# Optimization experiments

Measured on AMD Instinct MI355X. Metric: run time of the kernel, lower is better.

Reference implementation:

```python
import jax, jax.numpy as jnp
import numpy as np

NU, NI = 100000, 50000      # global embedding table sizes
U, I = 50000, 20000         # nodes in this subgraph
E = 400000                  # edges per direction
HID, H = 512, 8
D = HID // H                # out_feats per head = 64
NEG_SLOPE = 0.2


def setup_inputs() -> dict:
    key = jax.random.key(0)
    ks = jax.random.split(key, 16)
    s = 1.0 / np.sqrt(HID)
    a = 1.0 / np.sqrt(D)
    return {
        'u_gid': jax.random.randint(ks[0], (U,), 0, NU),
        'i_gid': jax.random.randint(ks[1], (I,), 0, NI),
        'src_u': jax.random.randint(ks[2], (E,), 0, U),
        'dst_i': jax.random.randint(ks[3], (E,), 0, I),
        'user_emb': jax.random.normal(ks[4], (NU, HID), jnp.float32) * 0.02,
        'item_emb': jax.random.normal(ks[5], (NI, HID), jnp.float32) * 0.02,
        # 'interact' (user -> item) GATConv params
        'W_ui': jax.random.normal(ks[6], (HID, HID), jnp.float32) * s,
        'al_ui': jax.random.normal(ks[7], (H, D), jnp.float32) * a,
        'ar_ui': jax.random.normal(ks[8], (H, D), jnp.float32) * a,
        'b_ui': jnp.zeros((HID,), jnp.float32),
        # 'interact_rev' (item -> user) GATConv params
        'W_iu': jax.random.normal(ks[9], (HID, HID), jnp.float32) * s,
        'al_iu': jax.random.normal(ks[10], (H, D), jnp.float32) * a,
        'ar_iu': jax.random.normal(ks[11], (H, D), jnp.float32) * a,
        'b_iu': jnp.zeros((HID,), jnp.float32),
    }


def gat_conv(h_src, h_dst, src, dst, W, attn_l, attn_r, bias, n_dst):
    """DGL GATConv (eval mode, allow_zero_in_degree): [n_dst, H, D]."""
    fs = (h_src @ W).reshape(-1, H, D)            # [Ns,H,D]
    fd = (h_dst @ W).reshape(-1, H, D)            # [Nd,H,D]
    el = jnp.sum(fs * attn_l, axis=-1)            # [Ns,H]
    er = jnp.sum(fd * attn_r, axis=-1)            # [Nd,H]
    e = jax.nn.leaky_relu(el[src] + er[dst], NEG_SLOPE)   # [E,H]
    # segment softmax over incoming edges of each destination
    emax = jax.ops.segment_max(e, dst, num_segments=n_dst)[dst]
    ex = jnp.exp(e - emax)                        # [E,H]
    denom = jax.ops.segment_sum(ex, dst, num_segments=n_dst)[dst]
    alpha = ex / denom                            # [E,H]
    msg = fs[src] * alpha[:, :, None]             # [E,H,D]
    out = jax.ops.segment_sum(msg, dst, num_segments=n_dst)  # zero for isolated dst
    return out + bias.reshape(1, H, D)


def reference(u_gid, i_gid, src_u, dst_i, user_emb, item_emb,
              W_ui, al_ui, ar_ui, b_ui, W_iu, al_iu, ar_iu, b_iu):
    h_u0 = user_emb[u_gid]                        # [U,HID]
    h_i0 = item_emb[i_gid]                        # [I,HID]
    # 'interact': user -> item
    h_item = gat_conv(h_u0, h_i0, src_u, dst_i, W_ui, al_ui, ar_ui, b_ui, I)
    # 'interact_rev': item -> user (reversed edges)
    h_user = gat_conv(h_i0, h_u0, dst_i, src_u, W_iu, al_iu, ar_iu, b_iu, U)
    h_user = h_user.reshape(U, HID)
    h_item = h_item.reshape(I, HID)
    item_mean = jnp.mean(h_item, axis=0, keepdims=True)        # [1,HID]
    item_expand = jnp.broadcast_to(item_mean, (U, HID))
    return jnp.concatenate([h_user, item_expand], axis=1)      # [U, 2*HID]
```

## Files before the change

kernel.cpp:

```cpp
#include <hip/hip_runtime.h>
#include <hip/hip_bf16.h>
#include <stdint.h>

#define U_NODES 50000
#define I_NODES 20000
#define N_NODES 70000
#define M_PAD   70016
#define E_EDGES 400000
#define HID     512

typedef __attribute__((ext_vector_type(8))) short short8;
typedef __attribute__((ext_vector_type(4))) float floatx4;

static __device__ __forceinline__ uint16_t f2b(float f) {
    uint32_t x = __float_as_uint(f);
    x += 0x7fffu + ((x >> 16) & 1u);
    return (uint16_t)(x >> 16);
}
static __device__ __forceinline__ float b2f(short u) {
    return __uint_as_float(((uint32_t)(uint16_t)u) << 16);
}

__global__ void gather_cast(const int* __restrict__ u_gid, const int* __restrict__ i_gid,
                            const float* __restrict__ user_emb, const float* __restrict__ item_emb,
                            uint16_t* __restrict__ Xb)
{
    int t = blockIdx.x * 256 + threadIdx.x;
    int n = t >> 7;
    int j = (t & 127) << 2;
    uint2 o;
    if (n < N_NODES) {
        const float* src = (n < U_NODES) ? (user_emb + (size_t)u_gid[n] * HID)
                                         : (item_emb + (size_t)i_gid[n - U_NODES] * HID);
        float4 v = *(const float4*)(src + j);
        o.x = (uint32_t)f2b(v.x) | ((uint32_t)f2b(v.y) << 16);
        o.y = (uint32_t)f2b(v.z) | ((uint32_t)f2b(v.w) << 16);
    } else { o.x = 0u; o.y = 0u; }
    *(uint2*)(Xb + (size_t)n * HID + j) = o;
}

__global__ void prep_w(const float* __restrict__ Wui, const float* __restrict__ Wiu,
                       uint16_t* __restrict__ Wt)
{
    int t = blockIdx.x * 256 + threadIdx.x;
    int n = t >> 9, k = t & 511;
    float v = (n < 512) ? Wui[k * 512 + n] : Wiu[k * 512 + (n - 512)];
    Wt[(size_t)n * 512 + k] = f2b(v);
}

__global__ __launch_bounds__(256) void gemm_bf16(const uint16_t* __restrict__ Xb,
                                                 const uint16_t* __restrict__ Wt,
                                                 const float* __restrict__ al_ui, const float* __restrict__ ar_ui,
                                                 const float* __restrict__ al_iu, const float* __restrict__ ar_iu,
                                                 uint16_t* __restrict__ F,
                                                 float* __restrict__ ELui, float* __restrict__ ERui,
                                                 float* __restrict__ ELiu, float* __restrict__ ERiu)
{
    __shared__ __align__(16) uint16_t As[128 * 64];
    __shared__ __align__(16) uint16_t Bs[128 * 64];
    const int tid = threadIdx.x;
    const int wave = tid >> 6, lane = tid & 63;

    int bid = blockIdx.x;
    int x = bid & 7, ii = bid >> 3;
    int L = x * 547 + ii;
    const int m0 = (L >> 3) * 128;
    const int n0 = (L & 7) * 128;
    const int wm = (wave & 1) * 64;
    const int wn = (wave >> 1) * 64;

    const int rl = lane >> 3;
    const int sg8 = ((lane & 7) ^ rl) * 8;
    const uint16_t* gA[4]; const uint16_t* gB[4];
    uint16_t* lA[4]; uint16_t* lB[4];
    #pragma unroll
    for (int l = 0; l < 4; ++l) {
        int c = wave * 4 + l;
        gA[l] = Xb + (size_t)(m0 + c * 8 + rl) * HID + sg8;
        gB[l] = Wt + (size_t)(n0 + c * 8 + rl) * HID + sg8;
        lA[l] = As + c * 512;
        lB[l] = Bs + c * 512;
    }

    floatx4 zero = {0.f, 0.f, 0.f, 0.f};
    floatx4 acc[4][4];
    #pragma unroll
    for (int a = 0; a < 4; ++a)
        #pragma unroll
        for (int b = 0; b < 4; ++b) acc[a][b] = zero;

    const int r = lane & 15, quad = lane >> 4;
    const int rx = r & 7;

    for (int k0 = 0; k0 < HID; k0 += 64) {
        __syncthreads();
        #pragma unroll
        for (int l = 0; l < 4; ++l) {
            __builtin_amdgcn_global_load_lds((const __attribute__((address_space(1))) void*)(gA[l] + k0),
                                             (__attribute__((address_space(3))) void*)lA[l], 16, 0, 0);
            __builtin_amdgcn_global_load_lds((const __attribute__((address_space(1))) void*)(gB[l] + k0),
                                             (__attribute__((address_space(3))) void*)lB[l], 16, 0, 0);
        }
        __syncthreads();
        #pragma unroll
        for (int ks = 0; ks < 2; ++ks) {
            short8 af[4], bf[4];
            #pragma unroll
            for (int tm = 0; tm < 4; ++tm) {
                int row = wm + tm * 16 + r;
                int sl = (ks * 4 + quad) ^ rx;
                af[tm] = *(const short8*)&As[row * 64 + sl * 8];
            }
            #pragma unroll
            for (int tn = 0; tn < 4; ++tn) {
                int row = wn + tn * 16 + r;
                int sl = (ks * 4 + quad) ^ rx;
                bf[tn] = *(const short8*)&Bs[row * 64 + sl * 8];
            }
            #pragma unroll
            for (int tm = 0; tm < 4; ++tm)
                #pragma unroll
                for (int tn = 0; tn < 4; ++tn)
                    acc[tm][tn] = __builtin_amdgcn_mfma_f32_16x16x32_bf16(af[tm], bf[tn], acc[tm][tn], 0, 0, 0);
        }
    }

    #pragma unroll
    for (int tm = 0; tm < 4; ++tm) {
        #pragma unroll
        for (int rr = 0; rr < 4; ++rr) {
            int row = m0 + wm + tm * 16 + quad * 4 + rr;
            if (row < N_NODES) {
                #pragma unroll
                for (int tn = 0; tn < 4; ++tn) {
                    int col = n0 + wn + tn * 16 + r;
                    F[(size_t)row * 1024 + col] = f2b(acc[tm][tn][rr]);
                }
            }
        }
    }

    int colh = n0 + wn;
    bool is_ui = colh < 512;
    int h = (colh & 511) >> 6;
    const float* alv = is_ui ? al_ui : al_iu;
    const float* arv = is_ui ? ar_ui : ar_iu;
    float* ELp = is_ui ? ELui : ELiu;
    float* ERp = is_ui ? ERui : ERiu;
    float al4[4], ar4[4];
    #pragma unroll
    for (int tn = 0; tn < 4; ++tn) {
        al4[tn] = alv[h * 64 + tn * 16 + r];
        ar4[tn] = arv[h * 64 + tn * 16 + r];
    }
    #pragma unroll
    for (int tm = 0; tm < 4; ++tm) {
        #pragma unroll
        for (int rr = 0; rr < 4; ++rr) {
            float sl = 0.f, sr = 0.f;
            #pragma unroll
            for (int tn = 0; tn < 4; ++tn) {
                sl += acc[tm][tn][rr] * al4[tn];
                sr += acc[tm][tn][rr] * ar4[tn];
            }
            #pragma unroll
            for (int d = 1; d < 16; d <<= 1) {
                sl += __shfl_xor(sl, d);
                sr += __shfl_xor(sr, d);
            }
            if (r == 0) {
                int row = m0 + wm + tm * 16 + quad * 4 + rr;
                if (row < N_NODES) {
                    ELp[row * 8 + h] = sl;
                    ERp[row * 8 + h] = sr;
                }
            }
        }
    }
}

__global__ void hist_kernel(const int* __restrict__ src_u, const int* __restrict__ dst_i,
                            int* __restrict__ counts_i, int* __restrict__ counts_u)
{
    int e = blockIdx.x * 256 + threadIdx.x;
    if (e >= E_EDGES) return;
    atomicAdd(&counts_i[dst_i[e]], 1);
    atomicAdd(&counts_u[src_u[e]], 1);
}

__global__ __launch_bounds__(1024) void scan_kernel(const int* __restrict__ counts_i,
                                                    const int* __restrict__ counts_u,
                                                    int* __restrict__ offs_i, int* __restrict__ cur_i,
                                                    int* __restrict__ offs_u, int* __restrict__ cur_u)
{
    const int* counts; int n; int* offs; int* cur;
    if (blockIdx.x == 0) { counts = counts_i; n = I_NODES; offs = offs_i; cur = cur_i; }
    else                 { counts = counts_u; n = U_NODES; offs = offs_u; cur = cur_u; }
    __shared__ int wsum[16];
    int tid = threadIdx.x, lane = tid & 63, w = tid >> 6;
    int carry = 0;
    for (int base = 0; base < n; base += 1024) {
        int i = base + tid;
        int v = (i < n) ? counts[i] : 0;
        int x = v;
        #pragma unroll
        for (int d = 1; d < 64; d <<= 1) {
            int y = __shfl_up(x, d, 64);
            if (lane >= d) x += y;
        }
        if (lane == 63) wsum[w] = x;
        __syncthreads();
        if (w == 0) {
            int s = (lane < 16) ? wsum[lane] : 0;
            #pragma unroll
            for (int d = 1; d < 16; d <<= 1) {
                int y = __shfl_up(s, d, 16);
                if ((lane & 15) >= d) s += y;
            }
            if (lane < 16) wsum[lane] = s;
        }
        __syncthreads();
        int wexcl = (w == 0) ? 0 : wsum[w - 1];
        int excl = carry + wexcl + (x - v);
        if (i < n) { offs[i] = excl; cur[i] = excl; }
        int tot = wsum[15];
        __syncthreads();
        carry += tot;
    }
    if (tid == 0) offs[n] = carry;
}

__global__ void scatter_kernel(const int* __restrict__ src_u, const int* __restrict__ dst_i,
                               int* __restrict__ cur_i, int* __restrict__ cur_u,
                               int* __restrict__ sorted_ui, int* __restrict__ sorted_iu,
                               const float* __restrict__ ELui, const float* __restrict__ ERui,
                               const float* __restrict__ ELiu, const float* __restrict__ ERiu,
                               float* __restrict__ ex_ui, float* __restrict__ ex_iu)
{
    int e = blockIdx.x * 256 + threadIdx.x;
    if (e >= E_EDGES) return;
    int s = src_u[e], d = dst_i[e];
    int dn = U_NODES + d;
    int p = atomicAdd(&cur_i[d], 1);
    int q = atomicAdd(&cur_u[s], 1);
    sorted_ui[p] = s;
    sorted_iu[q] = dn;
    #pragma unroll
    for (int h = 0; h < 8; ++h) {
        float e1 = ELui[s * 8 + h] + ERui[dn * 8 + h];
        e1 = (e1 >= 0.f) ? e1 : 0.2f * e1;
        ex_ui[(size_t)p * 8 + h] = __expf(e1);
        float e2 = ELiu[dn * 8 + h] + ERiu[s * 8 + h];
        e2 = (e2 >= 0.f) ? e2 : 0.2f * e2;
        ex_iu[(size_t)q * 8 + h] = __expf(e2);
    }
}

#define IBLK ((I_NODES + 3) / 4)
#define UBLK ((U_NODES + 3) / 4)
__global__ __launch_bounds__(256) void agg3_kernel(
    const int* __restrict__ offs_i, const int* __restrict__ sorted_ui, const float* __restrict__ ex_ui,
    const int* __restrict__ offs_u, const int* __restrict__ sorted_iu, const float* __restrict__ ex_iu,
    const uint16_t* __restrict__ F, const float* __restrict__ b_iu,
    float* __restrict__ out, float* __restrict__ itemF)
{
    int bid = blockIdx.x;
    int w = threadIdx.x >> 6, lane = threadIdx.x & 63;
    bool item_mode = bid < IBLK;
    const int* offs; const int* srcs; const float* ex; int dst, colbase, n_dst;
    if (item_mode) { offs = offs_i; srcs = sorted_ui; ex = ex_ui; dst = bid * 4 + w;          colbase = 0;   n_dst = I_NODES; }
    else           { offs = offs_u; srcs = sorted_iu; ex = ex_iu; dst = (bid - IBLK) * 4 + w; colbase = 512; n_dst = U_NODES; }
    if (dst >= n_dst) return;
    int h = lane >> 3;
    int j0 = offs[dst], j1 = offs[dst + 1];

    float den = 0.f;
    float acc[8] = {0.f, 0.f, 0.f, 0.f, 0.f, 0.f, 0.f, 0.f};
    const int fb = colbase + lane * 8;
    int j = j0;
    for (; j + 8 <= j1; j += 8) {
        int s[8]; float wt[8]; short8 f[8];
        #pragma unroll
        for (int i = 0; i < 8; ++i) s[i] = srcs[j + i];
        #pragma unroll
        for (int i = 0; i < 8; ++i) wt[i] = ex[(size_t)(j + i) * 8 + h];
        #pragma unroll
        for (int i = 0; i < 8; ++i) f[i] = *(const short8*)&F[(size_t)s[i] * 1024 + fb];
        #pragma unroll
        for (int i = 0; i < 8; ++i) {
            den += wt[i];
            #pragma unroll
            for (int q = 0; q < 8; ++q) acc[q] += wt[i] * b2f(f[i][q]);
        }
    }
    for (; j + 4 <= j1; j += 4) {
        int s[4]; float wt[4]; short8 f[4];
        #pragma unroll
        for (int i = 0; i < 4; ++i) s[i] = srcs[j + i];
        #pragma unroll
        for (int i = 0; i < 4; ++i) wt[i] = ex[(size_t)(j + i) * 8 + h];
        #pragma unroll
        for (int i = 0; i < 4; ++i) f[i] = *(const short8*)&F[(size_t)s[i] * 1024 + fb];
        #pragma unroll
        for (int i = 0; i < 4; ++i) {
            den += wt[i];
            #pragma unroll
            for (int q = 0; q < 8; ++q) acc[q] += wt[i] * b2f(f[i][q]);
        }
    }
    for (; j < j1; ++j) {
        int s0 = srcs[j];
        float w0 = ex[(size_t)j * 8 + h];
        short8 f0 = *(const short8*)&F[(size_t)s0 * 1024 + fb];
        den += w0;
        #pragma unroll
        for (int q = 0; q < 8; ++q) acc[q] += w0 * b2f(f0[q]);
    }
    float inv = (j1 > j0) ? (1.f / den) : 0.f;
    #pragma unroll
    for (int q = 0; q < 8; ++q) acc[q] *= inv;

    int col = lane * 8;
    if (item_mode) {
        float* o = itemF + (size_t)dst * 512 + col;
        float4 v0 = {acc[0], acc[1], acc[2], acc[3]};
        float4 v1 = {acc[4], acc[5], acc[6], acc[7]};
        *(float4*)(o + 0) = v0;
        *(float4*)(o + 4) = v1;
    } else {
        float* o = out + (size_t)dst * 1024 + col;
        float4 v0 = {acc[0] + b_iu[col + 0], acc[1] + b_iu[col + 1],
                     acc[2] + b_iu[col + 2], acc[3] + b_iu[col + 3]};
        float4 v1 = {acc[4] + b_iu[col + 4], acc[5] + b_iu[col + 5],
                     acc[6] + b_iu[col + 6], acc[7] + b_iu[col + 7]};
        *(float4*)(o + 0) = v0;
        *(float4*)(o + 4) = v1;
    }
}

__global__ void item_reduce(const float* __restrict__ itemF, float* __restrict__ partial2)
{
    int b = blockIdx.x;
    int t = threadIdx.x;
    int cg = (t & 127) * 4;
    int rp = t >> 7;
    float4 s = {0.f, 0.f, 0.f, 0.f};
    int r0 = b * 500;
    for (int r = r0 + rp; r < r0 + 500; r += 2) {
        float4 v = *(const float4*)&itemF[(size_t)r * 512 + cg];
        s.x += v.x; s.y += v.y; s.z += v.z; s.w += v.w;
    }
    *(float4*)&partial2[(size_t)(b * 2 + rp) * 512 + cg] = s;
}

__global__ void meanvec_kernel(const float* __restrict__ partial2, const float* __restrict__ b_ui,
                               float* __restrict__ mean_vec)
{
    int c = threadIdx.x;
    float s = 0.f;
    for (int p = 0; p < 80; ++p) s += partial2[p * 512 + c];
    mean_vec[c] = s * (1.0f / (float)I_NODES) + b_ui[c];
}

__global__ void bcast_kernel(const float* __restrict__ mean_vec, float* __restrict__ out)
{
    int t = blockIdx.x * 256 + threadIdx.x;
    int u = t >> 7, q = t & 127;
    float4 v = ((const float4*)mean_vec)[q];
    *(float4*)(out + (size_t)u * 1024 + 512 + q * 4) = v;
}

extern "C" void kernel_launch(void* const* d_in, const int* in_sizes, int n_in,
                              void* d_out, int out_size, void* d_ws, size_t ws_size,
                              hipStream_t stream)
{
    const int*   u_gid    = (const int*)d_in[0];
    const int*   i_gid    = (const int*)d_in[1];
    const int*   src_u    = (const int*)d_in[2];
    const int*   dst_i    = (const int*)d_in[3];
    const float* user_emb = (const float*)d_in[4];
    const float* item_emb = (const float*)d_in[5];
    const float* W_ui     = (const float*)d_in[6];
    const float* al_ui    = (const float*)d_in[7];
    const float* ar_ui    = (const float*)d_in[8];
    const float* b_ui     = (const float*)d_in[9];
    const float* W_iu     = (const float*)d_in[10];
    const float* al_iu    = (const float*)d_in[11];
    const float* ar_iu    = (const float*)d_in[12];
    const float* b_iu     = (const float*)d_in[13];
    float* out = (float*)d_out;

    char* ws = (char*)d_ws;
    size_t off = 0;
    auto alloc = [&](size_t bytes) -> void* {
        void* p = ws + off;
        off = (off + bytes + 255) & ~(size_t)255;
        return p;
    };
    uint16_t* Xb   = (uint16_t*)alloc((size_t)M_PAD * 512 * 2);
    uint16_t* Wt   = (uint16_t*)alloc((size_t)1024 * 512 * 2);
    uint16_t* F    = (uint16_t*)alloc((size_t)M_PAD * 1024 * 2);
    float* ELui    = (float*)alloc((size_t)N_NODES * 8 * 4);
    float* ERui    = (float*)alloc((size_t)N_NODES * 8 * 4);
    float* ELiu    = (float*)alloc((size_t)N_NODES * 8 * 4);
    float* ERiu    = (float*)alloc((size_t)N_NODES * 8 * 4);
    int* offs_i    = (int*)alloc((size_t)(I_NODES + 1) * 4);
    int* cur_i     = (int*)alloc((size_t)I_NODES * 4);
    int* offs_u    = (int*)alloc((size_t)(U_NODES + 1) * 4);
    int* cur_u     = (int*)alloc((size_t)U_NODES * 4);
    int* sorted_ui = (int*)alloc((size_t)E_EDGES * 4);
    int* sorted_iu = (int*)alloc((size_t)E_EDGES * 4);
    float* ex_ui   = (float*)alloc((size_t)E_EDGES * 8 * 4);
    float* ex_iu   = (float*)alloc((size_t)E_EDGES * 8 * 4);
    float* itemF   = (float*)alloc((size_t)I_NODES * 512 * 4);
    float* partial2= (float*)alloc((size_t)80 * 512 * 4);
    char* zptr = ws + off;
    int*   counts_i = (int*)alloc((size_t)I_NODES * 4);
    int*   counts_u = (int*)alloc((size_t)U_NODES * 4);
    size_t zbytes = (size_t)((ws + off) - zptr);
    float* mean_vec = (float*)alloc(512 * 4);
    (void)ws_size; (void)in_sizes; (void)n_in; (void)out_size;

    hipMemsetAsync(zptr, 0, zbytes, stream);
    prep_w<<<2048, 256, 0, stream>>>(W_ui, W_iu, Wt);
    gather_cast<<<M_PAD * 128 / 256, 256, 0, stream>>>(u_gid, i_gid, user_emb, item_emb, Xb);
    gemm_bf16<<<(M_PAD / 128) * 8, 256, 0, stream>>>(Xb, Wt, al_ui, ar_ui, al_iu, ar_iu,
                                                     F, ELui, ERui, ELiu, ERiu);
    hist_kernel<<<(E_EDGES + 255) / 256, 256, 0, stream>>>(src_u, dst_i, counts_i, counts_u);
    scan_kernel<<<2, 1024, 0, stream>>>(counts_i, counts_u, offs_i, cur_i, offs_u, cur_u);
    scatter_kernel<<<(E_EDGES + 255) / 256, 256, 0, stream>>>(src_u, dst_i, cur_i, cur_u,
                                                              sorted_ui, sorted_iu,
                                                              ELui, ERui, ELiu, ERiu,
                                                              ex_ui, ex_iu);
    agg3_kernel<<<IBLK + UBLK, 256, 0, stream>>>(offs_i, sorted_ui, ex_ui,
                                                 offs_u, sorted_iu, ex_iu,
                                                 F, b_iu, out, itemF);
    item_reduce<<<40, 256, 0, stream>>>(itemF, partial2);
    meanvec_kernel<<<1, 512, 0, stream>>>(partial2, b_ui, mean_vec);
    bcast_kernel<<<U_NODES * 128 / 256, 256, 0, stream>>>(mean_vec, out);
}
```

Before: 918.7 us.

## Double-buffer GEMM K-loop and skip unused feature/EL stores per tile

The GEMM main loop now uses two LDS buffers of half the K depth (32), so global-to-LDS loads for the next K slice are issued before computing on the current one, with one barrier per step instead of two. The epilogue stores bf16 features and EL only for row/column combinations that are actually consumed: user rows need W_ui features, item rows need W_iu. Tiles that are fully mismatched compute only ER. This aims to hide load latency and cut global write traffic, at the cost of a new swizzle and more synchronisation steps.

```diff
diff --git a/kernel.cpp b/kernel.cpp
--- a/kernel.cpp
+++ b/kernel.cpp
@@ -56,8 +56,8 @@
                                                  float* __restrict__ ELui, float* __restrict__ ERui,
                                                  float* __restrict__ ELiu, float* __restrict__ ERiu)
 {
-    __shared__ __align__(16) uint16_t As[128 * 64];
-    __shared__ __align__(16) uint16_t Bs[128 * 64];
+    __shared__ __align__(16) uint16_t As[2][128 * 32];
+    __shared__ __align__(16) uint16_t Bs[2][128 * 32];
     const int tid = threadIdx.x;
     const int wave = tid >> 6, lane = tid & 63;
 
@@ -69,18 +69,13 @@
     const int wm = (wave & 1) * 64;
     const int wn = (wave >> 1) * 64;
 
-    const int rl = lane >> 3;
-    const int sg8 = ((lane & 7) ^ rl) * 8;
-    const uint16_t* gA[4]; const uint16_t* gB[4];
-    uint16_t* lA[4]; uint16_t* lB[4];
-    #pragma unroll
-    for (int l = 0; l < 4; ++l) {
-        int c = wave * 4 + l;
-        gA[l] = Xb + (size_t)(m0 + c * 8 + rl) * HID + sg8;
-        gB[l] = Wt + (size_t)(n0 + c * 8 + rl) * HID + sg8;
-        lA[l] = As + c * 512;
-        lB[l] = Bs + c * 512;
-    }
+    const int rl2 = lane >> 2;
+    const int sg = ((lane & 3) ^ ((lane >> 3) & 3)) * 8;
+    const int ca = wave * 2, cb = wave * 2 + 1;
+    const uint16_t* gA0 = Xb + (size_t)(m0 + ca * 16 + rl2) * HID + sg;
+    const uint16_t* gA1 = Xb + (size_t)(m0 + cb * 16 + rl2) * HID + sg;
+    const uint16_t* gB0 = Wt + (size_t)(n0 + ca * 16 + rl2) * HID + sg;
+    const uint16_t* gB1 = Wt + (size_t)(n0 + cb * 16 + rl2) * HID + sg;
 
     floatx4 zero = {0.f, 0.f, 0.f, 0.f};
     floatx4 acc[4][4];
@@ -90,90 +85,108 @@
         for (int b = 0; b < 4; ++b) acc[a][b] = zero;
 
     const int r = lane & 15, quad = lane >> 4;
-    const int rx = r & 7;
-
-    for (int k0 = 0; k0 < HID; k0 += 64) {
+    const int slq8 = (quad ^ ((r >> 1) & 3)) * 8;
+
+#define STAGE(KO, BUF) do {                                                                         \
+    __builtin_amdgcn_global_load_lds((const __attribute__((address_space(1))) void*)(gA0 + (KO)),   \
+                                     (__attribute__((address_space(3))) void*)(&As[BUF][ca * 512]), 16, 0, 0); \
+    __builtin_amdgcn_global_load_lds((const __attribute__((address_space(1))) void*)(gA1 + (KO)),   \
+                                     (__attribute__((address_space(3))) void*)(&As[BUF][cb * 512]), 16, 0, 0); \
+    __builtin_amdgcn_global_load_lds((const __attribute__((address_space(1))) void*)(gB0 + (KO)),   \
+                                     (__attribute__((address_space(3))) void*)(&Bs[BUF][ca * 512]), 16, 0, 0); \
+    __builtin_amdgcn_global_load_lds((const __attribute__((address_space(1))) void*)(gB1 + (KO)),   \
+                                     (__attribute__((address_space(3))) void*)(&Bs[BUF][cb * 512]), 16, 0, 0); \
+} while (0)
+
+#define COMPUTE(BUF) do {                                                                           \
+    short8 af[4], bf[4];                                                                            \
+    _Pragma("unroll")                                                                               \
+    for (int tm = 0; tm < 4; ++tm)                                                                  \
+        af[tm] = *(const short8*)&As[BUF][(wm + tm * 16 + r) * 32 + slq8];                          \
+    _Pragma("unroll")                                                                               \
+    for (int tn = 0; tn < 4; ++tn)                                                                  \
+        bf[tn] = *(const short8*)&Bs[BUF][(wn + tn * 16 + r) * 32 + slq8];                          \
+    _Pragma("unroll")                                                                               \
+    for (int tm = 0; tm < 4; ++tm)                                                                  \
+        _Pragma("unroll")                                                                           \
+        for (int tn = 0; tn < 4; ++tn)                                                              \
+            acc[tm][tn] = __builtin_amdgcn_mfma_f32_16x16x32_bf16(af[tm], bf[tn], acc[tm][tn], 0, 0, 0); \
+} while (0)
+
+    STAGE(0, 0);
+    __syncthreads();
+    #pragma unroll
+    for (int t = 0; t < 15; ++t) {
+        const int bc = t & 1;
+        STAGE((t + 1) * 32, bc ^ 1);
+        COMPUTE(bc);
         __syncthreads();
-        #pragma unroll
-        for (int l = 0; l < 4; ++l) {
-            __builtin_amdgcn_global_load_lds((const __attribute__((address_space(1))) void*)(gA[l] + k0),
-                                             (__attribute__((address_space(3))) void*)lA[l], 16, 0, 0);
-            __builtin_amdgcn_global_load_lds((const __attribute__((address_space(1))) void*)(gB[l] + k0),
-                                             (__attribute__((address_space(3))) void*)lB[l], 16, 0, 0);
-        }
-        __syncthreads();
-        #pragma unroll
-        for (int ks = 0; ks < 2; ++ks) {
-            short8 af[4], bf[4];
+    }
+    COMPUTE(1);
+
+#undef STAGE
+#undef COMPUTE
+
+    const bool collo = (n0 < 512);
+    const bool allU = (m0 + 128 <= U_NODES);
+    const bool allI = (m0 >= U_NODES);
+    const bool storeb = (allU && collo) || (allI && !collo) || (!allU && !allI);
+
+    const int colh = n0 + wn;
+    const int h = (colh & 511) >> 6;
+    const float* arv = collo ? ar_ui : ar_iu;
+    float* ERp = collo ? ERui : ERiu;
+    float ar4[4];
+    #pragma unroll
+    for (int tn = 0; tn < 4; ++tn) ar4[tn] = arv[h * 64 + tn * 16 + r];
+
+    if (storeb) {
+        const float* alv = collo ? al_ui : al_iu;
+        float* ELp = collo ? ELui : ELiu;
+        float al4[4];
+        #pragma unroll
+        for (int tn = 0; tn < 4; ++tn) al4[tn] = alv[h * 64 + tn * 16 + r];
+        #pragma unroll
+        for (int tm = 0; tm < 4; ++tm) {
             #pragma unroll
-            for (int tm = 0; tm < 4; ++tm) {
-                int row = wm + tm * 16 + r;
-                int sl = (ks * 4 + quad) ^ rx;
-                af[tm] = *(const short8*)&As[row * 64 + sl * 8];
-            }
-            #pragma unroll
-            for (int tn = 0; tn < 4; ++tn) {
-                int row = wn + tn * 16 + r;
-                int sl = (ks * 4 + quad) ^ rx;
-                bf[tn] = *(const short8*)&Bs[row * 64 + sl * 8];
-            }
-            #pragma unroll
-            for (int tm = 0; tm < 4; ++tm)
-                #pragma unroll
-                for (int tn = 0; tn < 4; ++tn)
-                    acc[tm][tn] = __builtin_amdgcn_mfma_f32_16x16x32_bf16(af[tm], bf[tn], acc[tm][tn], 0, 0, 0);
-        }
-    }
-
-    #pragma unroll
-    for (int tm = 0; tm < 4; ++tm) {
-        #pragma unroll
-        for (int rr = 0; rr < 4; ++rr) {
-            int row = m0 + wm + tm * 16 + quad * 4 + rr;
-            if (row < N_NODES) {
+            for (int rr = 0; rr < 4; ++rr) {
+                int row = m0 + wm + tm * 16 + quad * 4 + rr;
+                float sl = 0.f, sr = 0.f;
                 #pragma unroll
                 for (int tn = 0; tn < 4; ++tn) {
-                    int col = n0 + wn + tn * 16 + r;
-                    F[(size_t)row * 1024 + col] = f2b(acc[tm][tn][rr]);
+                    sl += acc[tm][tn][rr] * al4[tn];
+                    sr += acc[tm][tn][rr] * ar4[tn];
                 }
-            }
-        }
-    }
-
-    int colh = n0 + wn;
-    bool is_ui = colh < 512;
-    int h = (colh & 511) >> 6;
-    const float* alv = is_ui ? al_ui : al_iu;
-    const float* arv = is_ui ? ar_ui : ar_iu;
-    float* ELp = is_ui ? ELui : ELiu;
-    float* ERp = is_ui ? ERui : ERiu;
-    float al4[4], ar4[4];
-    #pragma unroll
-    for (int tn = 0; tn < 4; ++tn) {
-        al4[tn] = alv[h * 64 + tn * 16 + r];
-        ar4[tn] = arv[h * 64 + tn * 16 + r];
-    }
-    #pragma unroll
-    for (int tm = 0; tm < 4; ++tm) {
-        #pragma unroll
-        for (int rr = 0; rr < 4; ++rr) {
-            float sl = 0.f, sr = 0.f;
-            #pragma unroll
-            for (int tn = 0; tn < 4; ++tn) {
-                sl += acc[tm][tn][rr] * al4[tn];
-                sr += acc[tm][tn][rr] * ar4[tn];
-            }
-            #pragma unroll
-            for (int d = 1; d < 16; d <<= 1) {
-                sl += __shfl_xor(sl, d);
-                sr += __shfl_xor(sr, d);
-            }
-            if (r == 0) {
-                int row = m0 + wm + tm * 16 + quad * 4 + rr;
-                if (row < N_NODES) {
+                if (row < N_NODES && ((row < U_NODES) == collo)) {
+                    #pragma unroll
+                    for (int tn = 0; tn < 4; ++tn) {
+                        int col = n0 + wn + tn * 16 + r;
+                        F[(size_t)row * 1024 + col] = f2b(acc[tm][tn][rr]);
+                    }
+                }
+                #pragma unroll
+                for (int d = 1; d < 16; d <<= 1) {
+                    sl += __shfl_xor(sl, d);
+                    sr += __shfl_xor(sr, d);
+                }
+                if (r == 0 && row < N_NODES) {
                     ELp[row * 8 + h] = sl;
                     ERp[row * 8 + h] = sr;
                 }
+            }
+        }
+    } else {
+        #pragma unroll
+        for (int tm = 0; tm < 4; ++tm) {
+            #pragma unroll
+            for (int rr = 0; rr < 4; ++rr) {
+                int row = m0 + wm + tm * 16 + quad * 4 + rr;
+                float sr = 0.f;
+                #pragma unroll
+                for (int tn = 0; tn < 4; ++tn) sr += acc[tm][tn][rr] * ar4[tn];
+                #pragma unroll
+                for (int d = 1; d < 16; d <<= 1) sr += __shfl_xor(sr, d);
+                if (r == 0 && row < N_NODES) ERp[row * 8 + h] = sr;
             }
         }
     }
```

Result: faster. 880.1 us (-4.2%).
